# Kernel optimization log

Hardware: AMD Instinct MI355X
Metric: run time of the kernel (lower is better)

## Reference

```python
import jax, jax.numpy as jnp
import numpy as np

N = 50000
E = 800000
EPS = 1e-5
# per-layer (in_dim, heads, out_dim, concat) matching GraphEncoder defaults
LAYERS = [(16, 4, 32, True), (128, 4, 32, True), (128, 4, 32, True), (128, 1, 128, False)]


def setup_inputs() -> dict:
    key = jax.random.key(0)
    ks = jax.random.split(key, 32)
    rn = lambda k, shape: jax.random.normal(k, shape, jnp.float32) * 0.1
    inp = {}
    inp["node_types"] = jax.random.randint(ks[0], (N,), 0, 3)
    inp["edge_index"] = jax.random.randint(ks[1], (2, E), 0, N)
    inp["emb"] = rn(ks[2], (3, 16))
    i = 3
    for li, (ind, h, od, _) in enumerate(LAYERS):
        inp[f"Wl{li}"] = rn(ks[i], (ind, h * od)); i += 1
        inp[f"Wr{li}"] = rn(ks[i], (ind, h * od)); i += 1
        inp[f"att{li}"] = rn(ks[i], (h, od)); i += 1
        inp[f"b{li}"] = rn(ks[i], (h * od if li < 3 else od,)); i += 1
    inp["ln_g"] = jnp.ones((4, 128), jnp.float32)
    inp["ln_b"] = jnp.zeros((4, 128), jnp.float32)
    return inp


def gatv2_layer(x, src, dst, Wl, Wr, att, b, heads, out_dim, concat):
    # PyG GATv2Conv (share_weights=False, negative_slope=0.2, self-loops added by caller)
    n = x.shape[0]
    xl = (x @ Wl).reshape(n, heads, out_dim)  # source transform (messages)
    xr = (x @ Wr).reshape(n, heads, out_dim)  # target transform
    e = jax.nn.leaky_relu(xl[src] + xr[dst], 0.2)          # [E', H, D]
    logit = jnp.einsum('ehd,hd->eh', e, att)               # [E', H]
    lmax = jax.ops.segment_max(logit, dst, num_segments=n)  # segment softmax over dst
    p = jnp.exp(logit - lmax[dst])
    z = jax.ops.segment_sum(p, dst, num_segments=n)
    alpha = p / z[dst]                                      # every node has a self-loop -> z > 0
    out = jax.ops.segment_sum(xl[src] * alpha[..., None], dst, num_segments=n)  # [n, H, D]
    out = out.reshape(n, heads * out_dim) if concat else out.mean(axis=1)
    return out + b


def layer_norm(x, g, b):
    mu = x.mean(-1, keepdims=True)
    var = ((x - mu) ** 2).mean(-1, keepdims=True)
    return (x - mu) / jnp.sqrt(var + EPS) * g + b


def reference(node_types, edge_index, emb, Wl0, Wr0, att0, b0, Wl1, Wr1, att1, b1,
              Wl2, Wr2, att2, b2, Wl3, Wr3, att3, b3, ln_g, ln_b):
    n = node_types.shape[0]
    loops = jnp.arange(n)
    src = jnp.concatenate([edge_index[0], loops])
    dst = jnp.concatenate([edge_index[1], loops])
    x = emb[node_types]
    params = [(Wl0, Wr0, att0, b0), (Wl1, Wr1, att1, b1), (Wl2, Wr2, att2, b2), (Wl3, Wr3, att3, b3)]
    for li, ((Wl, Wr, att, b), (_, h, od, concat)) in enumerate(zip(params, LAYERS)):
        res = x
        x = gatv2_layer(x, src, dst, Wl, Wr, att, b, h, od, concat)
        if x.shape[-1] == res.shape[-1]:
            x = x + res
        x = jax.nn.relu(layer_norm(x, ln_g[li], ln_b[li]))
    return x
```

## Files before the change

kernel.cpp:

```cpp
#include <hip/hip_runtime.h>

__global__ void GraphEncoder_20555713479231_kernel() {}

using hfrag8 = __attribute__((ext_vector_type(8))) _Float16;
using facc4  = __attribute__((ext_vector_type(4))) float;
using h2     = __attribute__((ext_vector_type(2))) _Float16;

__device__ __forceinline__ unsigned short f2h_bits(float f) {
  union { _Float16 h; unsigned short u; } c;
  c.h = (_Float16)f;
  return c.u;
}
__device__ __forceinline__ unsigned packh(float a, float b) {
  return (unsigned)f2h_bits(a) | ((unsigned)f2h_bits(b) << 16);
}
__device__ __forceinline__ h2 u2h(unsigned u) {
  union { unsigned u; h2 h; } c;
  c.u = u;
  return c.h;
}
__device__ __forceinline__ unsigned h22u(h2 h) {
  union { h2 h; unsigned u; } c;
  c.h = h;
  return c.u;
}
__device__ __forceinline__ float h2f_lo(unsigned u) { return (float)u2h(u).x; }
__device__ __forceinline__ float h2f_hi(unsigned u) { return (float)u2h(u).y; }

#define LOG2E 1.4426950408889634f

__global__ __launch_bounds__(256) void k_hist(const int* __restrict__ src,
                                              const int* __restrict__ dst,
                                              const int* __restrict__ types,
                                              int* __restrict__ deg,
                                              unsigned* __restrict__ h01, int e) {
  int i = blockIdx.x * blockDim.x + threadIdx.x;
  if (i >= e) return;
  int d = dst[i];
  atomicAdd(&deg[d], 1);
  int ty = types[src[i]] & 3;
  if (ty < 2) atomicAdd(&h01[d], ty == 0 ? 1u : 65536u);
}

__global__ __launch_bounds__(256) void k_scan1(const int* __restrict__ deg,
                                               int* __restrict__ off,
                                               int* __restrict__ bsum, int n) {
  __shared__ int wsum[4];
  int tid = threadIdx.x;
  int gid = blockIdx.x * 256 + tid;
  int lane = tid & 63, wid = tid >> 6;
  int v = (gid < n) ? (deg[gid] + 1) : 0;
  int x = v;
  #pragma unroll
  for (int d = 1; d < 64; d <<= 1) {
    int t = __shfl_up(x, d);
    if (lane >= d) x += t;
  }
  if (lane == 63) wsum[wid] = x;
  __syncthreads();
  int wpre = 0;
  for (int k = 0; k < wid; ++k) wpre += wsum[k];
  if (gid < n) off[gid] = wpre + x - v;
  if (tid == 0) {
    int t = 0;
    #pragma unroll
    for (int k = 0; k < 4; ++k) t += wsum[k];
    bsum[blockIdx.x] = t;
  }
}

__global__ __launch_bounds__(256) void k_scan23(int* __restrict__ off,
                                                const int* __restrict__ bsum,
                                                int* __restrict__ pos,
                                                int* __restrict__ csr, int nb, int n) {
  __shared__ int sh[8];
  int tid = threadIdx.x, lane = tid & 63, wid = tid >> 6;
  int p = 0, t = 0;
  for (int k = tid; k < nb; k += 256) {
    int bv = bsum[k];
    t += bv;
    if (k < (int)blockIdx.x) p += bv;
  }
  #pragma unroll
  for (int d = 1; d < 64; d <<= 1) {
    p += __shfl_xor(p, d);
    t += __shfl_xor(t, d);
  }
  if (lane == 0) { sh[wid] = p; sh[4 + wid] = t; }
  __syncthreads();
  p = sh[0] + sh[1] + sh[2] + sh[3];
  t = sh[4] + sh[5] + sh[6] + sh[7];
  int gid = blockIdx.x * 256 + tid;
  if (gid < n) {
    int o = off[gid] + p;
    off[gid] = o;
    csr[o] = gid;
    pos[gid] = o + 1;
  }
  if (blockIdx.x == 0) {
    if (tid == 0) off[n] = t;
    if (tid < 16) csr[t + tid] = 0;
  }
}

__global__ __launch_bounds__(256) void k_fill(const int* __restrict__ src,
                                              const int* __restrict__ dst,
                                              int* __restrict__ pos,
                                              int* __restrict__ csr, int e) {
  int i = blockIdx.x * blockDim.x + threadIdx.x;
  if (i < e) {
    int d = dst[i];
    int p = atomicAdd(&pos[d], 1);
    csr[p] = src[i];
  }
}

__global__ __launch_bounds__(256)
void k_pack3(const float* __restrict__ wl1, const float* __restrict__ wr1,
             const float* __restrict__ wl2, const float* __restrict__ wr2,
             const float* __restrict__ wl3, const float* __restrict__ wr3,
             const float* __restrict__ emb,
             const float* __restrict__ wl0, const float* __restrict__ wr0,
             const float* __restrict__ att0, int n,
             unsigned short* __restrict__ bp,
             unsigned* __restrict__ tlb, float* __restrict__ w0tab,
             int* __restrict__ deg, unsigned* __restrict__ h01) {
  int b = blockIdx.x;
  if (b < 384) {
    int idx = b * 256 + threadIdx.x;
    int layer = idx >> 15;
    int r = idx & 32767;
    int j = r & 7, lane = (r >> 3) & 63, ct = (r >> 9) & 15, t = r >> 13;
    int k = t * 32 + (lane >> 4) * 8 + j;
    int c = ct * 16 + (lane & 15);
    const float* wl = (layer == 0) ? wl1 : ((layer == 1) ? wl2 : wl3);
    const float* wr = (layer == 0) ? wr1 : ((layer == 1) ? wr2 : wr3);
    float v = (c < 128) ? wl[k * 128 + c] : wr[k * 128 + (c - 128)];
    bp[idx] = f2h_bits(v);
  } else if (b == 384) {
    __shared__ float stl[384], str[384];
    int tid = threadIdx.x;
    if (tid < 192) {
      int row = tid >> 6, cp = tid & 63, c0 = cp * 2;
      float al0 = 0.f, al1 = 0.f, ar0 = 0.f, ar1 = 0.f;
      #pragma unroll
      for (int k = 0; k < 16; ++k) {
        float ev = emb[row * 16 + k];
        al0 += ev * wl0[k * 128 + c0];
        al1 += ev * wl0[k * 128 + c0 + 1];
        ar0 += ev * wr0[k * 128 + c0];
        ar1 += ev * wr0[k * 128 + c0 + 1];
      }
      tlb[row * 64 + cp] = packh(al0, al1);
      stl[row * 128 + c0] = al0; stl[row * 128 + c0 + 1] = al1;
      str[row * 128 + c0] = ar0; str[row * 128 + c0 + 1] = ar1;
    }
    __syncthreads();
    if (tid < 192) {
      int tyv = tid >> 6, lane = tid & 63, f0 = lane * 2;
      float xr0 = str[tyv * 128 + f0], xr1 = str[tyv * 128 + f0 + 1];
      float a0 = att0[f0] * LOG2E, a1 = att0[f0 + 1] * LOG2E;
      #pragma unroll
      for (int ty = 0; ty < 3; ++ty) {
        float x0 = stl[ty * 128 + f0], x1 = stl[ty * 128 + f0 + 1];
        float t0 = x0 + xr0; t0 = t0 > 0.f ? t0 : 0.2f * t0;
        float t1 = x1 + xr1; t1 = t1 > 0.f ? t1 : 0.2f * t1;
        float c = t0 * a0 + t1 * a1;
        c += __shfl_xor(c, 1);
        c += __shfl_xor(c, 2);
        c += __shfl_xor(c, 4);
        c += __shfl_xor(c, 8);
        if ((lane & 15) == 0)
          w0tab[(tyv * 3 + ty) * 4 + (lane >> 4)] = __builtin_amdgcn_exp2f(c);
      }
    }
  } else {
    int i = (b - 385) * 256 + threadIdx.x;
    if (i < n) { deg[i] = 0; h01[i] = 0u; }
  }
}

__global__ __launch_bounds__(256)
void k_agg0h(const int* __restrict__ off, const unsigned* __restrict__ h01,
             const int* __restrict__ types,
             const unsigned* __restrict__ tlb, const float* __restrict__ w0tab,
             const float* __restrict__ bias,
             const float* __restrict__ lng, const float* __restrict__ lnb,
             unsigned* __restrict__ yout, int n) {
  int v = (blockIdx.x * blockDim.x + threadIdx.x) >> 6;
  int lane = threadIdx.x & 63;
  if (v >= n) return;
  v = __builtin_amdgcn_readfirstlane(v);
  int beg = off[v], end = off[v + 1];
  int m = end - beg;
  unsigned hc = h01[v];
  int tyv = types[v] & 3;
  float cnt[3];
  int c0 = (int)(hc & 0xffffu), c1 = (int)(hc >> 16);
  cnt[0] = (float)c0;
  cnt[1] = (float)c1;
  cnt[2] = (float)((m - 1) - c0 - c1);
  cnt[tyv] += 1.f;
  int head = lane >> 4;
  int f0 = lane * 2;
  float s = 0.f, O0 = 0.f, O1 = 0.f;
  #pragma unroll
  for (int ty = 0; ty < 3; ++ty) {
    float w = cnt[ty] * w0tab[(tyv * 3 + ty) * 4 + head];
    unsigned p = tlb[ty * 64 + lane];
    s += w;
    O0 = fmaf(w, h2f_lo(p), O0);
    O1 = fmaf(w, h2f_hi(p), O1);
  }
  float inv = 1.f / s;
  float o0 = O0 * inv + bias[f0];
  float o1 = O1 * inv + bias[f0 + 1];
  float sum = o0 + o1, sq = o0 * o0 + o1 * o1;
  #pragma unroll
  for (int d2 = 1; d2 < 64; d2 <<= 1) {
    sum += __shfl_xor(sum, d2);
    sq += __shfl_xor(sq, d2);
  }
  float mu = sum * (1.f / 128.f);
  float var = sq * (1.f / 128.f) - mu * mu;
  float rstd = rsqrtf(var + 1e-5f);
  float y0 = fmaxf((o0 - mu) * rstd * lng[f0] + lnb[f0], 0.f);
  float y1 = fmaxf((o1 - mu) * rstd * lng[f0 + 1] + lnb[f0 + 1], 0.f);
  yout[(size_t)v * 64 + lane] = packh(y0, y1);
}

__global__ __launch_bounds__(256)
void k_gemm(const unsigned* __restrict__ x, const unsigned short* __restrict__ bp,
            unsigned* __restrict__ xlo, unsigned* __restrict__ xro, int nstrips, int n) {
  int wave = (blockIdx.x * 256 + threadIdx.x) >> 6;
  int lane = threadIdx.x & 63;
  if (wave >= nstrips) return;
  int r0 = wave * 16;
  int row = r0 + (lane & 15);
  if (row >= n) row = n - 1;
  int quad = lane >> 4;
  const unsigned* ap = x + (size_t)row * 64;
  hfrag8 a[4];
  #pragma unroll
  for (int t = 0; t < 4; ++t) a[t] = *(const hfrag8*)(ap + t * 16 + quad * 4);
  unsigned short* xloS = (unsigned short*)xlo;
  unsigned short* xroS = (unsigned short*)xro;
  int rbase = r0 + quad * 4;
  #pragma unroll
  for (int ct = 0; ct < 16; ++ct) {
    facc4 acc = {0.f, 0.f, 0.f, 0.f};
    #pragma unroll
    for (int t = 0; t < 4; ++t) {
      hfrag8 b = *(const hfrag8*)(bp + (size_t)(((t * 16 + ct) * 64 + lane) * 8));
      acc = __builtin_amdgcn_mfma_f32_16x16x32_f16(a[t], b, acc, 0, 0, 0);
    }
    int col = (ct & 7) * 16 + (lane & 15);
    unsigned short* dstp = (ct < 8) ? xloS : xroS;
    #pragma unroll
    for (int i = 0; i < 4; ++i) {
      int r = rbase + i;
      if (r < n) dstp[(size_t)r * 128 + col] = f2h_bits(acc[i]);
    }
  }
}

__global__ __launch_bounds__(256)
void k_agg(const int* __restrict__ off, const int* __restrict__ csr,
           const unsigned* __restrict__ xl, const unsigned* __restrict__ xr,
           const float* __restrict__ att, const float* __restrict__ bias,
           const unsigned* __restrict__ xres,
           const float* __restrict__ lng, const float* __restrict__ lnb,
           unsigned* __restrict__ ybf, float* __restrict__ yf32, int n, int wide) {
  int v = (blockIdx.x * blockDim.x + threadIdx.x) >> 6;
  int lane = threadIdx.x & 63;
  if (v >= n) return;
  v = __builtin_amdgcn_readfirstlane(v);
  int f0 = lane * 2;
  h2 a2;
  a2.x = (_Float16)(att[f0] * LOG2E);
  a2.y = (_Float16)(att[f0 + 1] * LOG2E);
  h2 r2 = u2h(xr[(size_t)v * 64 + lane]);
  h2 k02 = {(_Float16)0.2f, (_Float16)0.2f};
  int beg = off[v], end = off[v + 1];
  int last = end - 1;
  const unsigned* xlp = xl + lane;
  int iA = csr[beg];
  int iB = csr[min(beg + 1, last)];
  int iC = csr[min(beg + 2, last)];
  int iD = csr[min(beg + 3, last)];
  unsigned pA = xlp[(size_t)iA * 64];
  unsigned pB = xlp[(size_t)iB * 64];
  unsigned pC = xlp[(size_t)iC * 64];
  unsigned pD = xlp[(size_t)iD * 64];
  float sa = 0.f, sb = 0.f;
  h2 Oa = {(_Float16)0.f, (_Float16)0.f};
  h2 Ob = {(_Float16)0.f, (_Float16)0.f};
  for (int e = beg; e < end; e += 2) {
    int i4 = csr[min(e + 4, last)];
    int i5 = csr[min(e + 5, last)];
    unsigned p4 = xlp[(size_t)i4 * 64];
    unsigned p5 = xlp[(size_t)i5 * 64];
    h2 xa = u2h(pA), xb = u2h(pB);
    h2 ta = xa + r2;
    h2 tb = xb + r2;
    h2 la = __builtin_elementwise_max(ta, ta * k02);
    h2 lb = __builtin_elementwise_max(tb, tb * k02);
    h2 da = la * a2;
    h2 db = lb * a2;
    h2 cp;
    cp.x = da.x + da.y;
    cp.y = db.x + db.y;
    unsigned cu = h22u(cp);
    cu = h22u(u2h(cu) + u2h((unsigned)__shfl_xor((int)cu, 1)));
    cu = h22u(u2h(cu) + u2h((unsigned)__shfl_xor((int)cu, 2)));
    cu = h22u(u2h(cu) + u2h((unsigned)__shfl_xor((int)cu, 4)));
    cu = h22u(u2h(cu) + u2h((unsigned)__shfl_xor((int)cu, 8)));
    if (wide) {
      cu = h22u(u2h(cu) + u2h((unsigned)__shfl_xor((int)cu, 16)));
      cu = h22u(u2h(cu) + u2h((unsigned)__shfl_xor((int)cu, 32)));
    }
    h2 cf = u2h(cu);
    float wa = __builtin_amdgcn_exp2f((float)cf.x);
    float wb = (e + 1 < end) ? __builtin_amdgcn_exp2f((float)cf.y) : 0.f;
    sa += wa;
    sb += wb;
    _Float16 wah = (_Float16)wa;
    _Float16 wbh = (_Float16)wb;
    h2 wa2 = {wah, wah};
    h2 wb2 = {wbh, wbh};
    Oa = wa2 * xa + Oa;
    Ob = wb2 * xb + Ob;
    pA = pC; pB = pD; pC = p4; pD = p5;
  }
  float s = sa + sb;
  float O0 = (float)Oa.x + (float)Ob.x;
  float O1 = (float)Oa.y + (float)Ob.y;
  float inv = 1.f / s;
  float o0 = O0 * inv + bias[f0];
  float o1 = O1 * inv + bias[f0 + 1];
  if (xres) {
    unsigned rs = xres[(size_t)v * 64 + lane];
    o0 += h2f_lo(rs);
    o1 += h2f_hi(rs);
  }
  float sum = o0 + o1, sq = o0 * o0 + o1 * o1;
  #pragma unroll
  for (int d2 = 1; d2 < 64; d2 <<= 1) {
    sum += __shfl_xor(sum, d2);
    sq += __shfl_xor(sq, d2);
  }
  float mu = sum * (1.f / 128.f);
  float var = sq * (1.f / 128.f) - mu * mu;
  float rstd = rsqrtf(var + 1e-5f);
  float y0 = fmaxf((o0 - mu) * rstd * lng[f0] + lnb[f0], 0.f);
  float y1 = fmaxf((o1 - mu) * rstd * lng[f0 + 1] + lnb[f0 + 1], 0.f);
  if (yf32) {
    *(float2*)(yf32 + (size_t)v * 128 + f0) = make_float2(y0, y1);
  } else {
    ybf[(size_t)v * 64 + lane] = packh(y0, y1);
  }
}

extern "C" void kernel_launch(void* const* d_in, const int* in_sizes, int n_in,
                              void* d_out, int out_size, void* d_ws, size_t ws_size,
                              hipStream_t stream) {
  (void)n_in; (void)out_size; (void)ws_size;
  const int* node_types = (const int*)d_in[0];
  const int* edge_index = (const int*)d_in[1];
  const float* emb = (const float*)d_in[2];
  const float* Wl0 = (const float*)d_in[3];
  const float* Wr0 = (const float*)d_in[4];
  const float* att0 = (const float*)d_in[5];
  const float* b0 = (const float*)d_in[6];
  const float* Wl1 = (const float*)d_in[7];
  const float* Wr1 = (const float*)d_in[8];
  const float* att1 = (const float*)d_in[9];
  const float* b1 = (const float*)d_in[10];
  const float* Wl2 = (const float*)d_in[11];
  const float* Wr2 = (const float*)d_in[12];
  const float* att2 = (const float*)d_in[13];
  const float* b2 = (const float*)d_in[14];
  const float* Wl3 = (const float*)d_in[15];
  const float* Wr3 = (const float*)d_in[16];
  const float* att3 = (const float*)d_in[17];
  const float* b3 = (const float*)d_in[18];
  const float* lng = (const float*)d_in[19];
  const float* lnb = (const float*)d_in[20];

  int n = in_sizes[0];
  int e = in_sizes[1] / 2;
  const int* srcp = edge_index;
  const int* dstp = edge_index + e;
  int nblocks = (n + 255) / 256;

  char* wsp = (char*)d_ws;
  size_t ofs = 0;
  int* deg = (int*)(wsp + ofs); ofs += (((size_t)n * 4) + 255) & ~(size_t)255;
  int* off = (int*)(wsp + ofs); ofs += (((size_t)(n + 1) * 4) + 255) & ~(size_t)255;
  int* csr = (int*)(wsp + ofs); ofs += (((size_t)(e + n + 64) * 4) + 255) & ~(size_t)255;
  int* bsum = (int*)(wsp + ofs); ofs += (((size_t)nblocks * 4) + 255) & ~(size_t)255;
  unsigned* h01 = (unsigned*)(wsp + ofs); ofs += (((size_t)n * 4) + 255) & ~(size_t)255;
  unsigned* xlb = (unsigned*)(wsp + ofs); ofs += (((size_t)n * 64 * 4) + 255) & ~(size_t)255;
  unsigned* xrb = (unsigned*)(wsp + ofs); ofs += (((size_t)n * 64 * 4) + 255) & ~(size_t)255;
  unsigned* xcur = (unsigned*)(wsp + ofs); ofs += (((size_t)n * 64 * 4) + 255) & ~(size_t)255;
  unsigned short* bp = (unsigned short*)(wsp + ofs); ofs += 3 * 65536;
  unsigned* tlb = (unsigned*)(wsp + ofs); ofs += 1024;
  float* w0tab = (float*)(wsp + ofs); ofs += 256;
  int* pos = deg;

  int packGrid = 385 + nblocks;
  k_pack3<<<packGrid, 256, 0, stream>>>(Wl1, Wr1, Wl2, Wr2, Wl3, Wr3,
                                        emb, Wl0, Wr0, att0, n,
                                        bp, tlb, w0tab, deg, h01);
  k_hist<<<(e + 255) / 256, 256, 0, stream>>>(srcp, dstp, node_types, deg, h01, e);
  k_scan1<<<nblocks, 256, 0, stream>>>(deg, off, bsum, n);
  k_scan23<<<nblocks, 256, 0, stream>>>(off, bsum, pos, csr, nblocks, n);
  k_fill<<<(e + 255) / 256, 256, 0, stream>>>(srcp, dstp, pos, csr, e);

  int aggBlocks = (n * 64 + 255) / 256;

  k_agg0h<<<aggBlocks, 256, 0, stream>>>(off, h01, node_types, tlb, w0tab,
                                         b0, lng, lnb, xcur, n);

  int nstrips = (n + 15) / 16;
  int gemmBlocks = (nstrips + 3) / 4;

  k_gemm<<<gemmBlocks, 256, 0, stream>>>(xcur, bp, xlb, xrb, nstrips, n);
  k_agg<<<aggBlocks, 256, 0, stream>>>(off, csr, xlb, xrb, att1, b1, xcur,
                                       lng + 128, lnb + 128, xcur, (float*)0, n, 0);
  k_gemm<<<gemmBlocks, 256, 0, stream>>>(xcur, bp + 32768, xlb, xrb, nstrips, n);
  k_agg<<<aggBlocks, 256, 0, stream>>>(off, csr, xlb, xrb, att2, b2, xcur,
                                       lng + 256, lnb + 256, xcur, (float*)0, n, 0);
  k_gemm<<<gemmBlocks, 256, 0, stream>>>(xcur, bp + 65536, xlb, xrb, nstrips, n);
  k_agg<<<aggBlocks, 256, 0, stream>>>(off, csr, xlb, xrb, att3, b3, xcur,
                                       lng + 384, lnb + 384, (unsigned*)0, (float*)d_out, n, 1);
}
```

Baseline: 421.1 us.

## Split each node's edges across two waves and fuse CSR fill with layer-0 aggregation

The aggregation kernel now gives each destination node two wavefronts, each handling alternate pairs of edges with a deeper prefetch stride. The partial softmax sums and weighted features are combined through shared memory after a block barrier. This is meant to raise memory-level parallelism for high-degree gathers, at the cost of twice as many waves, an extra barrier and duplicated per-node setup loads. Separately, the CSR fill kernel and the layer-0 aggregation kernel are merged into one launch to save a launch. Layer-0 aggregation does not read csr, so running it alongside the fill is safe.

```diff
diff --git a/kernel.cpp b/kernel.cpp
--- a/kernel.cpp
+++ b/kernel.cpp
@@ -100,18 +100,6 @@
   if (blockIdx.x == 0) {
     if (tid == 0) off[n] = t;
     if (tid < 16) csr[t + tid] = 0;
-  }
-}
-
-__global__ __launch_bounds__(256) void k_fill(const int* __restrict__ src,
-                                              const int* __restrict__ dst,
-                                              int* __restrict__ pos,
-                                              int* __restrict__ csr, int e) {
-  int i = blockIdx.x * blockDim.x + threadIdx.x;
-  if (i < e) {
-    int d = dst[i];
-    int p = atomicAdd(&pos[d], 1);
-    csr[p] = src[i];
   }
 }
 
@@ -181,13 +169,25 @@
 }
 
 __global__ __launch_bounds__(256)
-void k_agg0h(const int* __restrict__ off, const unsigned* __restrict__ h01,
-             const int* __restrict__ types,
-             const unsigned* __restrict__ tlb, const float* __restrict__ w0tab,
-             const float* __restrict__ bias,
-             const float* __restrict__ lng, const float* __restrict__ lnb,
-             unsigned* __restrict__ yout, int n) {
-  int v = (blockIdx.x * blockDim.x + threadIdx.x) >> 6;
+void k_fill_agg0(const int* __restrict__ src, const int* __restrict__ dst,
+                 int* __restrict__ pos, int* __restrict__ csr, int e, int fillB,
+                 const int* __restrict__ off, const unsigned* __restrict__ h01,
+                 const int* __restrict__ types,
+                 const unsigned* __restrict__ tlb, const float* __restrict__ w0tab,
+                 const float* __restrict__ bias,
+                 const float* __restrict__ lng, const float* __restrict__ lnb,
+                 unsigned* __restrict__ yout, int n) {
+  int b = blockIdx.x;
+  if (b < fillB) {
+    int i = b * 256 + threadIdx.x;
+    if (i < e) {
+      int d = dst[i];
+      int p = atomicAdd(&pos[d], 1);
+      csr[p] = src[i];
+    }
+    return;
+  }
+  int v = ((b - fillB) * 256 + threadIdx.x) >> 6;
   int lane = threadIdx.x & 63;
   if (v >= n) return;
   v = __builtin_amdgcn_readfirstlane(v);
@@ -271,9 +271,13 @@
            const unsigned* __restrict__ xres,
            const float* __restrict__ lng, const float* __restrict__ lnb,
            unsigned* __restrict__ ybf, float* __restrict__ yf32, int n, int wide) {
-  int v = (blockIdx.x * blockDim.x + threadIdx.x) >> 6;
+  __shared__ float shs[2][64], shx[2][64], shy[2][64];
+  int gid = blockIdx.x * 256 + threadIdx.x;
+  int v = gid >> 7;
+  int p = (threadIdx.x >> 6) & 1;
+  int slot = threadIdx.x >> 7;
   int lane = threadIdx.x & 63;
-  if (v >= n) return;
+  if (v >= n) v = n - 1;
   v = __builtin_amdgcn_readfirstlane(v);
   int f0 = lane * 2;
   h2 a2;
@@ -284,22 +288,23 @@
   int beg = off[v], end = off[v + 1];
   int last = end - 1;
   const unsigned* xlp = xl + lane;
-  int iA = csr[beg];
-  int iB = csr[min(beg + 1, last)];
-  int iC = csr[min(beg + 2, last)];
-  int iD = csr[min(beg + 3, last)];
-  unsigned pA = xlp[(size_t)iA * 64];
-  unsigned pB = xlp[(size_t)iB * 64];
-  unsigned pC = xlp[(size_t)iC * 64];
-  unsigned pD = xlp[(size_t)iD * 64];
+  int e0 = beg + 2 * p;
+  int iA = csr[min(e0, last)];
+  int iB = csr[min(e0 + 1, last)];
+  int iC = csr[min(e0 + 4, last)];
+  int iD = csr[min(e0 + 5, last)];
+  unsigned pA = xlp[((unsigned)iA << 6)];
+  unsigned pB = xlp[((unsigned)iB << 6)];
+  unsigned pC = xlp[((unsigned)iC << 6)];
+  unsigned pD = xlp[((unsigned)iD << 6)];
   float sa = 0.f, sb = 0.f;
   h2 Oa = {(_Float16)0.f, (_Float16)0.f};
   h2 Ob = {(_Float16)0.f, (_Float16)0.f};
-  for (int e = beg; e < end; e += 2) {
-    int i4 = csr[min(e + 4, last)];
-    int i5 = csr[min(e + 5, last)];
-    unsigned p4 = xlp[(size_t)i4 * 64];
-    unsigned p5 = xlp[(size_t)i5 * 64];
+  for (int e = e0; e < end; e += 4) {
+    int i4 = csr[min(e + 8, last)];
+    int i5 = csr[min(e + 9, last)];
+    unsigned p4 = xlp[((unsigned)i4 << 6)];
+    unsigned p5 = xlp[((unsigned)i5 << 6)];
     h2 xa = u2h(pA), xb = u2h(pB);
     h2 ta = xa + r2;
     h2 tb = xb + r2;
@@ -333,11 +338,21 @@
     pA = pC; pB = pD; pC = p4; pD = p5;
   }
   float s = sa + sb;
-  float O0 = (float)Oa.x + (float)Ob.x;
-  float O1 = (float)Oa.y + (float)Ob.y;
+  float Ox = (float)Oa.x + (float)Ob.x;
+  float Oy = (float)Oa.y + (float)Ob.y;
+  if (p == 1) {
+    shs[slot][lane] = s;
+    shx[slot][lane] = Ox;
+    shy[slot][lane] = Oy;
+  }
+  __syncthreads();
+  if (p == 1) return;
+  s += shs[slot][lane];
+  Ox += shx[slot][lane];
+  Oy += shy[slot][lane];
   float inv = 1.f / s;
-  float o0 = O0 * inv + bias[f0];
-  float o1 = O1 * inv + bias[f0 + 1];
+  float o0 = Ox * inv + bias[f0];
+  float o1 = Oy * inv + bias[f0 + 1];
   if (xres) {
     unsigned rs = xres[(size_t)v * 64 + lane];
     o0 += h2f_lo(rs);
@@ -415,13 +430,14 @@
   k_hist<<<(e + 255) / 256, 256, 0, stream>>>(srcp, dstp, node_types, deg, h01, e);
   k_scan1<<<nblocks, 256, 0, stream>>>(deg, off, bsum, n);
   k_scan23<<<nblocks, 256, 0, stream>>>(off, bsum, pos, csr, nblocks, n);
-  k_fill<<<(e + 255) / 256, 256, 0, stream>>>(srcp, dstp, pos, csr, e);
-
-  int aggBlocks = (n * 64 + 255) / 256;
-
-  k_agg0h<<<aggBlocks, 256, 0, stream>>>(off, h01, node_types, tlb, w0tab,
-                                         b0, lng, lnb, xcur, n);
-
+
+  int fillB = (e + 255) / 256;
+  int agg0B = (n * 64 + 255) / 256;
+  k_fill_agg0<<<fillB + agg0B, 256, 0, stream>>>(srcp, dstp, pos, csr, e, fillB,
+                                                 off, h01, node_types, tlb, w0tab,
+                                                 b0, lng, lnb, xcur, n);
+
+  int aggBlocks = (n * 128 + 255) / 256;
   int nstrips = (n + 15) / 16;
   int gemmBlocks = (nstrips + 3) / 4;
 
```

Result: slower. 478.3 us (+13.6%).

## Pack degree and type counts into one atomic, fuse CSR fill with layer-0 aggregation, split GEMM

Applied to the files above, without the earlier changes.

Degree and the per-type source counts now share one 64-bit word, so the histogram issues one atomic per edge instead of two. The CSR fill kernel and the layer-0 aggregation run as one launch with disjoint block ranges, which removes a launch and lets the two overlap. This is valid because layer 0 only reads offsets and counts, not csr. The GEMM gives each 16-row strip two waves, one for the xl half and one for the xr half, doubling wave parallelism at the cost of loading the A fragments twice.

```diff
diff --git a/kernel.cpp b/kernel.cpp
--- a/kernel.cpp
+++ b/kernel.cpp
@@ -32,24 +32,30 @@
 __global__ __launch_bounds__(256) void k_hist(const int* __restrict__ src,
                                               const int* __restrict__ dst,
                                               const int* __restrict__ types,
-                                              int* __restrict__ deg,
-                                              unsigned* __restrict__ h01, int e) {
+                                              unsigned long long* __restrict__ dh,
+                                              int e) {
   int i = blockIdx.x * blockDim.x + threadIdx.x;
   if (i >= e) return;
   int d = dst[i];
-  atomicAdd(&deg[d], 1);
   int ty = types[src[i]] & 3;
-  if (ty < 2) atomicAdd(&h01[d], ty == 0 ? 1u : 65536u);
-}
-
-__global__ __launch_bounds__(256) void k_scan1(const int* __restrict__ deg,
+  unsigned long long add = 1ull;
+  if (ty == 0) add |= (1ull << 16);
+  else if (ty == 1) add |= (1ull << 32);
+  atomicAdd(&dh[d], add);
+}
+
+__global__ __launch_bounds__(256) void k_scan1(const unsigned long long* __restrict__ dh,
                                                int* __restrict__ off,
                                                int* __restrict__ bsum, int n) {
   __shared__ int wsum[4];
   int tid = threadIdx.x;
   int gid = blockIdx.x * 256 + tid;
   int lane = tid & 63, wid = tid >> 6;
-  int v = (gid < n) ? (deg[gid] + 1) : 0;
+  int v = 0;
+  if (gid < n) {
+    unsigned lo = ((const unsigned*)dh)[2 * gid];
+    v = (int)(lo & 0xffffu) + 1;
+  }
   int x = v;
   #pragma unroll
   for (int d = 1; d < 64; d <<= 1) {
@@ -103,18 +109,6 @@
   }
 }
 
-__global__ __launch_bounds__(256) void k_fill(const int* __restrict__ src,
-                                              const int* __restrict__ dst,
-                                              int* __restrict__ pos,
-                                              int* __restrict__ csr, int e) {
-  int i = blockIdx.x * blockDim.x + threadIdx.x;
-  if (i < e) {
-    int d = dst[i];
-    int p = atomicAdd(&pos[d], 1);
-    csr[p] = src[i];
-  }
-}
-
 __global__ __launch_bounds__(256)
 void k_pack3(const float* __restrict__ wl1, const float* __restrict__ wr1,
              const float* __restrict__ wl2, const float* __restrict__ wr2,
@@ -124,7 +118,7 @@
              const float* __restrict__ att0, int n,
              unsigned short* __restrict__ bp,
              unsigned* __restrict__ tlb, float* __restrict__ w0tab,
-             int* __restrict__ deg, unsigned* __restrict__ h01) {
+             unsigned long long* __restrict__ dh) {
   int b = blockIdx.x;
   if (b < 384) {
     int idx = b * 256 + threadIdx.x;
@@ -176,27 +170,41 @@
     }
   } else {
     int i = (b - 385) * 256 + threadIdx.x;
-    if (i < n) { deg[i] = 0; h01[i] = 0u; }
+    if (i < n) dh[i] = 0ull;
   }
 }
 
 __global__ __launch_bounds__(256)
-void k_agg0h(const int* __restrict__ off, const unsigned* __restrict__ h01,
-             const int* __restrict__ types,
-             const unsigned* __restrict__ tlb, const float* __restrict__ w0tab,
-             const float* __restrict__ bias,
-             const float* __restrict__ lng, const float* __restrict__ lnb,
-             unsigned* __restrict__ yout, int n) {
-  int v = (blockIdx.x * blockDim.x + threadIdx.x) >> 6;
+void k_fill_agg0(const int* __restrict__ src, const int* __restrict__ dst,
+                 int* __restrict__ pos, int* __restrict__ csr, int e, int fillB,
+                 const int* __restrict__ off,
+                 const unsigned long long* __restrict__ dh,
+                 const int* __restrict__ types,
+                 const unsigned* __restrict__ tlb, const float* __restrict__ w0tab,
+                 const float* __restrict__ bias,
+                 const float* __restrict__ lng, const float* __restrict__ lnb,
+                 unsigned* __restrict__ yout, int n) {
+  int b = blockIdx.x;
+  if (b < fillB) {
+    int i = b * 256 + threadIdx.x;
+    if (i < e) {
+      int d = dst[i];
+      int p = atomicAdd(&pos[d], 1);
+      csr[p] = src[i];
+    }
+    return;
+  }
+  int v = ((b - fillB) * 256 + threadIdx.x) >> 6;
   int lane = threadIdx.x & 63;
   if (v >= n) return;
   v = __builtin_amdgcn_readfirstlane(v);
   int beg = off[v], end = off[v + 1];
   int m = end - beg;
-  unsigned hc = h01[v];
+  unsigned lo = ((const unsigned*)dh)[2 * v];
+  unsigned hi = ((const unsigned*)dh)[2 * v + 1];
   int tyv = types[v] & 3;
   float cnt[3];
-  int c0 = (int)(hc & 0xffffu), c1 = (int)(hc >> 16);
+  int c0 = (int)(lo >> 16), c1 = (int)(hi & 0xffffu);
   cnt[0] = (float)c0;
   cnt[1] = (float)c1;
   cnt[2] = (float)((m - 1) - c0 - c1);
@@ -234,8 +242,10 @@
             unsigned* __restrict__ xlo, unsigned* __restrict__ xro, int nstrips, int n) {
   int wave = (blockIdx.x * 256 + threadIdx.x) >> 6;
   int lane = threadIdx.x & 63;
-  if (wave >= nstrips) return;
-  int r0 = wave * 16;
+  if (wave >= 2 * nstrips) return;
+  int strip = wave >> 1;
+  int half = wave & 1;
+  int r0 = strip * 16;
   int row = r0 + (lane & 15);
   if (row >= n) row = n - 1;
   int quad = lane >> 4;
@@ -243,23 +253,23 @@
   hfrag8 a[4];
   #pragma unroll
   for (int t = 0; t < 4; ++t) a[t] = *(const hfrag8*)(ap + t * 16 + quad * 4);
-  unsigned short* xloS = (unsigned short*)xlo;
-  unsigned short* xroS = (unsigned short*)xro;
+  unsigned short* dstS = half ? (unsigned short*)xro : (unsigned short*)xlo;
   int rbase = r0 + quad * 4;
-  #pragma unroll
-  for (int ct = 0; ct < 16; ++ct) {
+  int ct0 = half * 8;
+  #pragma unroll
+  for (int cc = 0; cc < 8; ++cc) {
+    int ct = ct0 + cc;
     facc4 acc = {0.f, 0.f, 0.f, 0.f};
     #pragma unroll
     for (int t = 0; t < 4; ++t) {
       hfrag8 b = *(const hfrag8*)(bp + (size_t)(((t * 16 + ct) * 64 + lane) * 8));
       acc = __builtin_amdgcn_mfma_f32_16x16x32_f16(a[t], b, acc, 0, 0, 0);
     }
-    int col = (ct & 7) * 16 + (lane & 15);
-    unsigned short* dstp = (ct < 8) ? xloS : xroS;
+    int col = cc * 16 + (lane & 15);
     #pragma unroll
     for (int i = 0; i < 4; ++i) {
       int r = rbase + i;
-      if (r < n) dstp[(size_t)r * 128 + col] = f2h_bits(acc[i]);
+      if (r < n) dstS[(size_t)r * 128 + col] = f2h_bits(acc[i]);
     }
   }
 }
@@ -395,35 +405,36 @@
 
   char* wsp = (char*)d_ws;
   size_t ofs = 0;
-  int* deg = (int*)(wsp + ofs); ofs += (((size_t)n * 4) + 255) & ~(size_t)255;
+  unsigned long long* dh = (unsigned long long*)(wsp + ofs);
+  ofs += (((size_t)n * 8) + 255) & ~(size_t)255;
+  int* pos = (int*)(wsp + ofs); ofs += (((size_t)n * 4) + 255) & ~(size_t)255;
   int* off = (int*)(wsp + ofs); ofs += (((size_t)(n + 1) * 4) + 255) & ~(size_t)255;
   int* csr = (int*)(wsp + ofs); ofs += (((size_t)(e + n + 64) * 4) + 255) & ~(size_t)255;
   int* bsum = (int*)(wsp + ofs); ofs += (((size_t)nblocks * 4) + 255) & ~(size_t)255;
-  unsigned* h01 = (unsigned*)(wsp + ofs); ofs += (((size_t)n * 4) + 255) & ~(size_t)255;
   unsigned* xlb = (unsigned*)(wsp + ofs); ofs += (((size_t)n * 64 * 4) + 255) & ~(size_t)255;
   unsigned* xrb = (unsigned*)(wsp + ofs); ofs += (((size_t)n * 64 * 4) + 255) & ~(size_t)255;
   unsigned* xcur = (unsigned*)(wsp + ofs); ofs += (((size_t)n * 64 * 4) + 255) & ~(size_t)255;
   unsigned short* bp = (unsigned short*)(wsp + ofs); ofs += 3 * 65536;
   unsigned* tlb = (unsigned*)(wsp + ofs); ofs += 1024;
   float* w0tab = (float*)(wsp + ofs); ofs += 256;
-  int* pos = deg;
 
   int packGrid = 385 + nblocks;
   k_pack3<<<packGrid, 256, 0, stream>>>(Wl1, Wr1, Wl2, Wr2, Wl3, Wr3,
                                         emb, Wl0, Wr0, att0, n,
-                                        bp, tlb, w0tab, deg, h01);
-  k_hist<<<(e + 255) / 256, 256, 0, stream>>>(srcp, dstp, node_types, deg, h01, e);
-  k_scan1<<<nblocks, 256, 0, stream>>>(deg, off, bsum, n);
+                                        bp, tlb, w0tab, dh);
+  k_hist<<<(e + 255) / 256, 256, 0, stream>>>(srcp, dstp, node_types, dh, e);
+  k_scan1<<<nblocks, 256, 0, stream>>>(dh, off, bsum, n);
   k_scan23<<<nblocks, 256, 0, stream>>>(off, bsum, pos, csr, nblocks, n);
-  k_fill<<<(e + 255) / 256, 256, 0, stream>>>(srcp, dstp, pos, csr, e);
+
+  int fillB = (e + 255) / 256;
+  int agg0B = (n * 64 + 255) / 256;
+  k_fill_agg0<<<fillB + agg0B, 256, 0, stream>>>(srcp, dstp, pos, csr, e, fillB,
+                                                 off, dh, node_types, tlb, w0tab,
+                                                 b0, lng, lnb, xcur, n);
 
   int aggBlocks = (n * 64 + 255) / 256;
-
-  k_agg0h<<<aggBlocks, 256, 0, stream>>>(off, h01, node_types, tlb, w0tab,
-                                         b0, lng, lnb, xcur, n);
-
   int nstrips = (n + 15) / 16;
-  int gemmBlocks = (nstrips + 3) / 4;
+  int gemmBlocks = (2 * nstrips + 3) / 4;
 
   k_gemm<<<gemmBlocks, 256, 0, stream>>>(xcur, bp, xlb, xrb, nstrips, n);
   k_agg<<<aggBlocks, 256, 0, stream>>>(off, csr, xlb, xrb, att1, b1, xcur,
```

Measured after the change: 406.8 us. 3.4% less time.
